# Optimization experiments

Measured on AMD Instinct MI355X. Metric: run time of the kernel, lower is better.

## Reference

```python
import jax, jax.numpy as jnp
import numpy as np

LN_EPS = 1e-5
BOUNDARY_ID = 0  # boundary_ids = {space_id} = {0}


def setup_inputs() -> dict:
    key = jax.random.key(0)
    k1, k2, k3 = jax.random.split(key, 3)
    B, T, D = 16, 8192, 256
    x = jax.random.normal(k1, (B, T, D), dtype=jnp.float32)
    input_ids = jax.random.randint(k2, (B, T), 0, 8, dtype=jnp.int64)
    W_proj = jax.random.normal(k3, (D, D), dtype=jnp.float32) / np.sqrt(D)
    b_proj = jnp.zeros((D,), dtype=jnp.float32)
    gamma = jnp.ones((D,), dtype=jnp.float32)
    beta = jnp.zeros((D,), dtype=jnp.float32)
    return {"x": x, "input_ids": input_ids, "W_proj": W_proj,
            "b_proj": b_proj, "gamma": gamma, "beta": beta}


def _pool(x, input_ids):
    # Boundary-defined segment mean pooling, vectorized via segment_sum.
    B, T, D = x.shape
    boundary = input_ids == BOUNDARY_ID                       # [B,T]
    nonb = ~boundary
    # A segment starts at a non-boundary token at t=0 or right after a boundary.
    prev_is_b = jnp.concatenate(
        [jnp.ones((B, 1), dtype=bool), boundary[:, :-1]], axis=1)
    start = nonb & prev_is_b
    seg = jnp.cumsum(start.astype(jnp.int32), axis=1) - 1     # seg idx per token
    MAXW = T  # static upper bound on number of segments (jit-safe padding)
    row_off = jnp.arange(B, dtype=jnp.int32)[:, None] * MAXW
    dump = B * MAXW  # boundary tokens go to a dummy segment, dropped below
    flat_ids = jnp.where(nonb, seg + row_off, dump).reshape(-1)
    sums = jax.ops.segment_sum(x.reshape(-1, D), flat_ids,
                               num_segments=B * MAXW + 1)[:-1]
    counts = jax.ops.segment_sum(jnp.ones((B * T,), x.dtype), flat_ids,
                                 num_segments=B * MAXW + 1)[:-1]
    sums = sums.reshape(B, MAXW, D)
    counts = counts.reshape(B, MAXW)
    mask = (counts > 0).astype(x.dtype)                       # [B,MAXW]
    padded = sums / jnp.maximum(counts, 1.0)[..., None]       # zeros where empty
    return padded, mask


def reference(x, input_ids, W_proj, b_proj, gamma, beta):
    padded, mask = _pool(x, input_ids)
    out = jnp.einsum('bwd,ed->bwe', padded, W_proj) + b_proj  # nn.Linear
    mu = jnp.mean(out, axis=-1, keepdims=True)
    var = jnp.mean(jnp.square(out - mu), axis=-1, keepdims=True)
    out = (out - mu) * jax.lax.rsqrt(var + LN_EPS) * gamma + beta
    return out, mask
```

## Files before the change

### kernel.cpp

```cpp
#include <hip/hip_runtime.h>
#include <hip/hip_bf16.h>
#include <math.h>

#define BB 16
#define TT 8192
#define DD 256
#define MAXSEG 4096
#define RPB 8
#define LN_EPS 1e-5f

typedef float vfloat4 __attribute__((ext_vector_type(4)));

__global__ __launch_bounds__(1024) void setup_kernel(
    const int* __restrict__ ids, const float* __restrict__ W,
    const float* __restrict__ bp, const float* __restrict__ gamma,
    const float* __restrict__ beta, int* __restrict__ counts,
    int* __restrict__ seg_start, int* __restrict__ nseg_g,
    float* __restrict__ mask_out, float* __restrict__ Wt,
    float* __restrict__ ln_empty) {
    __shared__ int wtot_s[16];
    __shared__ int wtot_n[16];
    __shared__ int segs[MAXSEG];
    __shared__ int pvals[MAXSEG];

    int tid = threadIdx.x;
    int lane = tid & 63;
    int wv = tid >> 6;

    if (blockIdx.x >= BB) {
        int bi = blockIdx.x - BB;
        if (bi < 64) {
            int d = bi * 4 + (tid >> 8);
            int e = tid & 255;
            Wt[d * DD + e] = W[e * DD + d];
        } else if (wv == 0) {
            int e0 = lane * 4;
            float4 v = *(const float4*)(bp + e0);
            float s = v.x + v.y + v.z + v.w;
            float sq = v.x * v.x + v.y * v.y + v.z * v.z + v.w * v.w;
#pragma unroll
            for (int o = 32; o > 0; o >>= 1) {
                s += __shfl_down(s, o);
                sq += __shfl_down(sq, o);
            }
            s = __shfl(s, 0);
            sq = __shfl(sq, 0);
            float mu = s * (1.f / (float)DD);
            float var = sq * (1.f / (float)DD) - mu * mu;
            float rs = rsqrtf(fmaxf(var, 0.f) + LN_EPS);
            float4 ge = *(const float4*)(gamma + e0);
            float4 be = *(const float4*)(beta + e0);
            float4 o4;
            o4.x = (v.x - mu) * rs * ge.x + be.x;
            o4.y = (v.y - mu) * rs * ge.y + be.y;
            o4.z = (v.z - mu) * rs * ge.z + be.z;
            o4.w = (v.w - mu) * rs * ge.w + be.w;
            *(float4*)(ln_empty + e0) = o4;
        }
        return;
    }

    const int TPT = 8;
    int b = blockIdx.x;
    const int* row = ids + b * TT;
    int t0 = tid * TPT;

    int4 q0 = ((const int4*)(row + t0))[0];
    int4 q1 = ((const int4*)(row + t0))[1];
    int v[TPT] = {q0.x, q0.y, q0.z, q0.w, q1.x, q1.y, q1.z, q1.w};
    int prev = (tid == 0) ? 0 : row[t0 - 1];

    bool nb[TPT], st[TPT];
    int cstart = 0, cnon = 0;
#pragma unroll
    for (int j = 0; j < TPT; ++j) {
        nb[j] = (v[j] != 0);
        int pv = (j == 0) ? prev : v[j - 1];
        st[j] = nb[j] && (pv == 0);
        cstart += st[j] ? 1 : 0;
        cnon += nb[j] ? 1 : 0;
    }

    int ss = cstart, sn = cnon;
#pragma unroll
    for (int o = 1; o < 64; o <<= 1) {
        int us = __shfl_up(ss, o);
        int un = __shfl_up(sn, o);
        if (lane >= o) { ss += us; sn += un; }
    }
    if (lane == 63) { wtot_s[wv] = ss; wtot_n[wv] = sn; }
    __syncthreads();

    int bs = 0, bn = 0, tot_s = 0, tot_n = 0;
#pragma unroll
    for (int j = 0; j < 16; ++j) {
        int a = wtot_s[j], c = wtot_n[j];
        if (j < wv) { bs += a; bn += c; }
        tot_s += a; tot_n += c;
    }
    bs += ss - cstart;
    bn += sn - cnon;

#pragma unroll
    for (int j = 0; j < TPT; ++j) {
        if (st[j]) { segs[bs] = t0 + j; pvals[bs] = bn; bs++; }
        bn += nb[j] ? 1 : 0;
    }
    __syncthreads();

    int ns = tot_s;
    for (int w = tid; w < TT; w += 1024) {
        int c = 0;
        if (w < ns) {
            int pe = (w + 1 < ns) ? pvals[w + 1] : tot_n;
            c = pe - pvals[w];
            seg_start[b * TT + w] = segs[w];
        }
        counts[b * TT + w] = c;
        mask_out[b * TT + w] = (w < ns) ? 1.0f : 0.0f;
    }
    if (tid == 0) nseg_g[b] = ns;
}

__global__ __launch_bounds__(256) void fused_kernel(
    const float* __restrict__ x, const float* __restrict__ Wt,
    const float* __restrict__ bp, const float* __restrict__ gamma,
    const float* __restrict__ beta, const int* __restrict__ counts,
    const int* __restrict__ seg_start, const int* __restrict__ nseg,
    const float* __restrict__ ln_e, float* __restrict__ out) {
    __shared__ float pooled[RPB][DD];
    __shared__ float red[4][RPB][2];

    int b = blockIdx.x;
    int wbase = blockIdx.y * RPB;
    int ns = nseg[b];
    int tid = threadIdx.x;
    int lane = tid & 63;
    int wv = tid >> 6;
    size_t rowbase = ((size_t)(b * TT + wbase)) * DD;

    if (wbase >= ns) {
        vfloat4 lv = *(const vfloat4*)(ln_e + 4 * lane);
        float* o = out + rowbase + 4 * lane;
#pragma unroll
        for (int rr = 0; rr < 2; ++rr) {
            int row = wv * 2 + rr;
            __builtin_nontemporal_store(lv, (vfloat4*)(o + (size_t)row * DD));
        }
        return;
    }
    int nr = min(RPB, ns - wbase);

#pragma unroll
    for (int rr = 0; rr < 2; ++rr) {
        int row = wv * 2 + rr;
        vfloat4 r = {0.f, 0.f, 0.f, 0.f};
        if (row < nr) {
            int w = wbase + row;
            int s = seg_start[b * TT + w];
            int len = counts[b * TT + w];
            const vfloat4* xp =
                (const vfloat4*)(x + ((size_t)(b * TT + s)) * DD) + lane;
            vfloat4 a[8];
#pragma unroll
            for (int j = 0; j < 8; ++j) a[j] = (vfloat4){0.f, 0.f, 0.f, 0.f};
            int t = 0;
            for (; t + 8 <= len; t += 8) {
#pragma unroll
                for (int j = 0; j < 8; ++j)
                    a[j] += __builtin_nontemporal_load(xp + (t + j) * 64);
            }
#pragma unroll
            for (int j = 0; j < 7; ++j)
                if (t + j < len)
                    a[j] += __builtin_nontemporal_load(xp + (t + j) * 64);
            r = ((a[0] + a[1]) + (a[2] + a[3])) + ((a[4] + a[5]) + (a[6] + a[7]));
            r *= (1.f / (float)len);
        }
        *(vfloat4*)&pooled[row][lane * 4] = r;
    }
    __syncthreads();

    int c = wv * 64 + lane;
    float acc[RPB];
    float bias = bp[c];
#pragma unroll
    for (int r = 0; r < RPB; ++r) acc[r] = bias;

    const float* Wc = Wt + c;
    float w0 = Wc[0 * DD];
    float w1 = Wc[1 * DD];
    float w2 = Wc[2 * DD];
    float w3 = Wc[3 * DD];
#pragma unroll 1
    for (int d0 = 0; d0 < DD; d0 += 4) {
        int dn = (d0 + 4) & 255;
        float n0 = Wc[(dn + 0) * DD];
        float n1 = Wc[(dn + 1) * DD];
        float n2 = Wc[(dn + 2) * DD];
        float n3 = Wc[(dn + 3) * DD];
#pragma unroll
        for (int r = 0; r < RPB; ++r) {
            const float4 p = *(const float4*)&pooled[r][d0];
            acc[r] = fmaf(p.x, w0, acc[r]);
            acc[r] = fmaf(p.y, w1, acc[r]);
            acc[r] = fmaf(p.z, w2, acc[r]);
            acc[r] = fmaf(p.w, w3, acc[r]);
        }
        w0 = n0; w1 = n1; w2 = n2; w3 = n3;
    }

#pragma unroll
    for (int r = 0; r < RPB; ++r) {
        float s = acc[r];
        float sq = acc[r] * acc[r];
#pragma unroll
        for (int o = 32; o > 0; o >>= 1) {
            s += __shfl_down(s, o);
            sq += __shfl_down(sq, o);
        }
        if (lane == 0) { red[wv][r][0] = s; red[wv][r][1] = sq; }
    }
    __syncthreads();

    float ga = gamma[c], be = beta[c];
#pragma unroll
    for (int r = 0; r < RPB; ++r) {
        float s = red[0][r][0] + red[1][r][0] + red[2][r][0] + red[3][r][0];
        float sq = red[0][r][1] + red[1][r][1] + red[2][r][1] + red[3][r][1];
        float mu = s * (1.f / (float)DD);
        float var = sq * (1.f / (float)DD) - mu * mu;
        float rs = rsqrtf(fmaxf(var, 0.f) + LN_EPS);
        float v = (acc[r] - mu) * rs * ga + be;
        __builtin_nontemporal_store(v, out + rowbase + (size_t)r * DD + c);
    }
}

extern "C" void kernel_launch(void* const* d_in, const int* in_sizes, int n_in,
                              void* d_out, int out_size, void* d_ws, size_t ws_size,
                              hipStream_t stream) {
    const float* x = (const float*)d_in[0];
    const int* ids = (const int*)d_in[1];
    const float* W = (const float*)d_in[2];
    const float* bp = (const float*)d_in[3];
    const float* gamma = (const float*)d_in[4];
    const float* beta = (const float*)d_in[5];

    float* out = (float*)d_out;
    float* mask = out + (size_t)BB * TT * DD;

    char* ws = (char*)d_ws;
    int* counts = (int*)ws;
    int* seg_start = (int*)(ws + (size_t)BB * TT * 4);
    int* nseg = (int*)(ws + (size_t)2 * BB * TT * 4);
    float* Wt = (float*)(ws + (size_t)2 * BB * TT * 4 + 256);
    float* ln_e = Wt + DD * DD;

    hipLaunchKernelGGL(setup_kernel, dim3(BB + 64 + 1), dim3(1024), 0, stream,
                       ids, W, bp, gamma, beta, counts, seg_start, nseg, mask,
                       Wt, ln_e);
    hipLaunchKernelGGL(fused_kernel, dim3(BB, TT / RPB), dim3(256), 0, stream,
                       x, Wt, bp, gamma, beta, counts, seg_start, nseg, ln_e, out);
}
```

Baseline: 269.6 us.

## Split fused pool+GEMM kernel into separate pooling and GEMM kernels

Breaks the single fused kernel into a pooling/fill kernel that writes pooled rows to a workspace buffer and a GEMM+LayerNorm kernel that reads them back. The GEMM loop now reads pooled values straight from global memory with 8-wide W register blocking. If the workspace is too small, it falls back to fusing the pooling into the GEMM kernel. The aim is to separate the memory-bound pooling from the compute phase so that neither stalls the other. The cost is an extra kernel launch plus a round trip of the pooled data through global memory.

```diff
diff --git a/kernel.cpp b/kernel.cpp
--- a/kernel.cpp
+++ b/kernel.cpp
@@ -122,24 +122,20 @@
     if (tid == 0) nseg_g[b] = ns;
 }
 
-__global__ __launch_bounds__(256) void fused_kernel(
-    const float* __restrict__ x, const float* __restrict__ Wt,
-    const float* __restrict__ bp, const float* __restrict__ gamma,
-    const float* __restrict__ beta, const int* __restrict__ counts,
+__global__ __launch_bounds__(256) void pool_fill_kernel(
+    const float* __restrict__ x, const int* __restrict__ counts,
     const int* __restrict__ seg_start, const int* __restrict__ nseg,
-    const float* __restrict__ ln_e, float* __restrict__ out) {
-    __shared__ float pooled[RPB][DD];
-    __shared__ float red[4][RPB][2];
-
+    const float* __restrict__ ln_e, float* __restrict__ pooled,
+    float* __restrict__ out, int capW) {
     int b = blockIdx.x;
     int wbase = blockIdx.y * RPB;
     int ns = nseg[b];
     int tid = threadIdx.x;
     int lane = tid & 63;
     int wv = tid >> 6;
-    size_t rowbase = ((size_t)(b * TT + wbase)) * DD;
 
     if (wbase >= ns) {
+        size_t rowbase = ((size_t)(b * TT + wbase)) * DD;
         vfloat4 lv = *(const vfloat4*)(ln_e + 4 * lane);
         float* o = out + rowbase + 4 * lane;
 #pragma unroll
@@ -149,6 +145,7 @@
         }
         return;
     }
+    if (wbase + RPB > capW) return;
     int nr = min(RPB, ns - wbase);
 
 #pragma unroll
@@ -177,37 +174,105 @@
             r = ((a[0] + a[1]) + (a[2] + a[3])) + ((a[4] + a[5]) + (a[6] + a[7]));
             r *= (1.f / (float)len);
         }
-        *(vfloat4*)&pooled[row][lane * 4] = r;
-    }
-    __syncthreads();
-
-    int c = wv * 64 + lane;
+        *(vfloat4*)(pooled + ((size_t)b * capW + wbase + wv * 2 + rr) * DD +
+                    4 * lane) = r;
+    }
+}
+
+__global__ __launch_bounds__(256) void gemm_kernel(
+    const float* __restrict__ x, const float* __restrict__ Wt,
+    const float* __restrict__ bp, const float* __restrict__ gamma,
+    const float* __restrict__ beta, const int* __restrict__ counts,
+    const int* __restrict__ seg_start, const int* __restrict__ nseg,
+    const float* __restrict__ pooled, float* __restrict__ out, int capW) {
+    __shared__ float pl[RPB][DD];
+    __shared__ float red[4][RPB][2];
+
+    int b = blockIdx.x;
+    int wbase = blockIdx.y * RPB;
+    int ns = nseg[b];
+    if (wbase >= ns) return;
+    int tid = threadIdx.x;
+    int lane = tid & 63;
+    int wv = tid >> 6;
+    int nr = min(RPB, ns - wbase);
+    size_t rowbase = ((size_t)(b * TT + wbase)) * DD;
+
+    int c = tid;
+    float bias = bp[c];
     float acc[RPB];
-    float bias = bp[c];
 #pragma unroll
     for (int r = 0; r < RPB; ++r) acc[r] = bias;
 
-    const float* Wc = Wt + c;
-    float w0 = Wc[0 * DD];
-    float w1 = Wc[1 * DD];
-    float w2 = Wc[2 * DD];
-    float w3 = Wc[3 * DD];
+    if (wbase + RPB <= capW) {
+        const float* __restrict__ pr = pooled + ((size_t)b * capW + wbase) * DD;
+        const float* __restrict__ Wc = Wt + c;
 #pragma unroll 1
-    for (int d0 = 0; d0 < DD; d0 += 4) {
-        int dn = (d0 + 4) & 255;
-        float n0 = Wc[(dn + 0) * DD];
-        float n1 = Wc[(dn + 1) * DD];
-        float n2 = Wc[(dn + 2) * DD];
-        float n3 = Wc[(dn + 3) * DD];
-#pragma unroll
-        for (int r = 0; r < RPB; ++r) {
-            const float4 p = *(const float4*)&pooled[r][d0];
-            acc[r] = fmaf(p.x, w0, acc[r]);
-            acc[r] = fmaf(p.y, w1, acc[r]);
-            acc[r] = fmaf(p.z, w2, acc[r]);
-            acc[r] = fmaf(p.w, w3, acc[r]);
-        }
-        w0 = n0; w1 = n1; w2 = n2; w3 = n3;
+        for (int d0 = 0; d0 < DD; d0 += 8) {
+            float w[8];
+#pragma unroll
+            for (int j = 0; j < 8; ++j) w[j] = Wc[(d0 + j) * DD];
+#pragma unroll
+            for (int r = 0; r < RPB; ++r) {
+#pragma unroll
+                for (int j = 0; j < 8; ++j)
+                    acc[r] = fmaf(pr[r * DD + d0 + j], w[j], acc[r]);
+            }
+        }
+    } else {
+#pragma unroll
+        for (int rr = 0; rr < 2; ++rr) {
+            int row = wv * 2 + rr;
+            vfloat4 r = {0.f, 0.f, 0.f, 0.f};
+            if (row < nr) {
+                int w = wbase + row;
+                int s = seg_start[b * TT + w];
+                int len = counts[b * TT + w];
+                const vfloat4* xp =
+                    (const vfloat4*)(x + ((size_t)(b * TT + s)) * DD) + lane;
+                vfloat4 a[8];
+#pragma unroll
+                for (int j = 0; j < 8; ++j) a[j] = (vfloat4){0.f, 0.f, 0.f, 0.f};
+                int t = 0;
+                for (; t + 8 <= len; t += 8) {
+#pragma unroll
+                    for (int j = 0; j < 8; ++j)
+                        a[j] += __builtin_nontemporal_load(xp + (t + j) * 64);
+                }
+#pragma unroll
+                for (int j = 0; j < 7; ++j)
+                    if (t + j < len)
+                        a[j] += __builtin_nontemporal_load(xp + (t + j) * 64);
+                r = ((a[0] + a[1]) + (a[2] + a[3])) +
+                    ((a[4] + a[5]) + (a[6] + a[7]));
+                r *= (1.f / (float)len);
+            }
+            *(vfloat4*)&pl[row][lane * 4] = r;
+        }
+        __syncthreads();
+
+        const float* Wc = Wt + c;
+        float w0 = Wc[0 * DD];
+        float w1 = Wc[1 * DD];
+        float w2 = Wc[2 * DD];
+        float w3 = Wc[3 * DD];
+#pragma unroll 1
+        for (int d0 = 0; d0 < DD; d0 += 4) {
+            int dn = (d0 + 4) & 255;
+            float n0 = Wc[(dn + 0) * DD];
+            float n1 = Wc[(dn + 1) * DD];
+            float n2 = Wc[(dn + 2) * DD];
+            float n3 = Wc[(dn + 3) * DD];
+#pragma unroll
+            for (int r = 0; r < RPB; ++r) {
+                const float4 p = *(const float4*)&pl[r][d0];
+                acc[r] = fmaf(p.x, w0, acc[r]);
+                acc[r] = fmaf(p.y, w1, acc[r]);
+                acc[r] = fmaf(p.z, w2, acc[r]);
+                acc[r] = fmaf(p.w, w3, acc[r]);
+            }
+            w0 = n0; w1 = n1; w2 = n2; w3 = n3;
+        }
     }
 
 #pragma unroll
@@ -255,10 +320,20 @@
     int* nseg = (int*)(ws + (size_t)2 * BB * TT * 4);
     float* Wt = (float*)(ws + (size_t)2 * BB * TT * 4 + 256);
     float* ln_e = Wt + DD * DD;
+    float* pooled = ln_e + 256;
+    size_t base = (size_t)2 * BB * TT * 4 + 256 + (size_t)DD * DD * 4 + 1024;
+    size_t avail = (ws_size > base) ? (ws_size - base) : 0;
+    long capW = (long)(avail / ((size_t)BB * DD * 4));
+    if (capW > MAXSEG) capW = MAXSEG;
+    capW &= ~(long)(RPB - 1);
 
     hipLaunchKernelGGL(setup_kernel, dim3(BB + 64 + 1), dim3(1024), 0, stream,
                        ids, W, bp, gamma, beta, counts, seg_start, nseg, mask,
                        Wt, ln_e);
-    hipLaunchKernelGGL(fused_kernel, dim3(BB, TT / RPB), dim3(256), 0, stream,
-                       x, Wt, bp, gamma, beta, counts, seg_start, nseg, ln_e, out);
+    hipLaunchKernelGGL(pool_fill_kernel, dim3(BB, TT / RPB), dim3(256), 0,
+                       stream, x, counts, seg_start, nseg, ln_e, pooled, out,
+                       (int)capW);
+    hipLaunchKernelGGL(gemm_kernel, dim3(BB, MAXSEG / RPB), dim3(256), 0,
+                       stream, x, Wt, bp, gamma, beta, counts, seg_start, nseg,
+                       pooled, out, (int)capW);
 }
```

Result: slower. 307.6 us (+14.1%).

## Process 32 pooled rows per block to amortize projection weight reads

Applied to the files above, without the earlier changes.

The fused kernel now has one block in every group of four pool 32 segment rows and run the projection and LayerNorm on all of them. The other three blocks, whose rows are already covered, exit early. Each weight column loaded from L2 is reused across 32 rows instead of 8, which cuts the repeated full-matrix weight traffic. In exchange each thread holds 32 accumulators, which raises register pressure. Pooling parallelism also drops, since fewer active blocks serialize four pooling passes, and the launched grid still includes the idle blocks.

```diff
diff --git a/kernel.cpp b/kernel.cpp
--- a/kernel.cpp
+++ b/kernel.cpp
@@ -7,6 +7,7 @@
 #define DD 256
 #define MAXSEG 4096
 #define RPB 8
+#define LROWS 32
 #define LN_EPS 1e-5f
 
 typedef float vfloat4 __attribute__((ext_vector_type(4)));
@@ -128,8 +129,8 @@
     const float* __restrict__ beta, const int* __restrict__ counts,
     const int* __restrict__ seg_start, const int* __restrict__ nseg,
     const float* __restrict__ ln_e, float* __restrict__ out) {
-    __shared__ float pooled[RPB][DD];
-    __shared__ float red[4][RPB][2];
+    __shared__ float pooled[LROWS][DD];
+    __shared__ float red[LROWS][4][2];
 
     int b = blockIdx.x;
     int wbase = blockIdx.y * RPB;
@@ -137,9 +138,9 @@
     int tid = threadIdx.x;
     int lane = tid & 63;
     int wv = tid >> 6;
-    size_t rowbase = ((size_t)(b * TT + wbase)) * DD;
 
     if (wbase >= ns) {
+        size_t rowbase = ((size_t)(b * TT + wbase)) * DD;
         vfloat4 lv = *(const vfloat4*)(ln_e + 4 * lane);
         float* o = out + rowbase + 4 * lane;
 #pragma unroll
@@ -149,49 +150,56 @@
         }
         return;
     }
-    int nr = min(RPB, ns - wbase);
-
-#pragma unroll
-    for (int rr = 0; rr < 2; ++rr) {
-        int row = wv * 2 + rr;
-        vfloat4 r = {0.f, 0.f, 0.f, 0.f};
-        if (row < nr) {
-            int w = wbase + row;
-            int s = seg_start[b * TT + w];
-            int len = counts[b * TT + w];
-            const vfloat4* xp =
-                (const vfloat4*)(x + ((size_t)(b * TT + s)) * DD) + lane;
-            vfloat4 a[8];
-#pragma unroll
-            for (int j = 0; j < 8; ++j) a[j] = (vfloat4){0.f, 0.f, 0.f, 0.f};
-            int t = 0;
-            for (; t + 8 <= len; t += 8) {
-#pragma unroll
-                for (int j = 0; j < 8; ++j)
-                    a[j] += __builtin_nontemporal_load(xp + (t + j) * 64);
+    if (wbase & (LROWS - 1)) return;
+    int nr = min(LROWS, ns - wbase);
+
+#pragma unroll 1
+    for (int pr = 0; pr < 4; ++pr) {
+#pragma unroll
+        for (int rr = 0; rr < 2; ++rr) {
+            int row = wv * 8 + pr * 2 + rr;
+            vfloat4 r = {0.f, 0.f, 0.f, 0.f};
+            if (row < nr) {
+                int w = wbase + row;
+                int s = seg_start[b * TT + w];
+                int len = counts[b * TT + w];
+                const vfloat4* xp =
+                    (const vfloat4*)(x + ((size_t)(b * TT + s)) * DD) + lane;
+                vfloat4 a[8];
+#pragma unroll
+                for (int j = 0; j < 8; ++j) a[j] = (vfloat4){0.f, 0.f, 0.f, 0.f};
+                int t = 0;
+                for (; t + 8 <= len; t += 8) {
+#pragma unroll
+                    for (int j = 0; j < 8; ++j)
+                        a[j] += __builtin_nontemporal_load(xp + (t + j) * 64);
+                }
+#pragma unroll
+                for (int j = 0; j < 7; ++j)
+                    if (t + j < len)
+                        a[j] += __builtin_nontemporal_load(xp + (t + j) * 64);
+                r = ((a[0] + a[1]) + (a[2] + a[3])) +
+                    ((a[4] + a[5]) + (a[6] + a[7]));
+                r *= (1.f / (float)len);
             }
-#pragma unroll
-            for (int j = 0; j < 7; ++j)
-                if (t + j < len)
-                    a[j] += __builtin_nontemporal_load(xp + (t + j) * 64);
-            r = ((a[0] + a[1]) + (a[2] + a[3])) + ((a[4] + a[5]) + (a[6] + a[7]));
-            r *= (1.f / (float)len);
-        }
-        *(vfloat4*)&pooled[row][lane * 4] = r;
-    }
-    __syncthreads();
-
-    int c = wv * 64 + lane;
-    float acc[RPB];
-    float bias = bp[c];
-#pragma unroll
-    for (int r = 0; r < RPB; ++r) acc[r] = bias;
-
+            *(vfloat4*)&pooled[row][lane * 4] = r;
+        }
+    }
+
+    int c = tid;
     const float* Wc = Wt + c;
     float w0 = Wc[0 * DD];
     float w1 = Wc[1 * DD];
     float w2 = Wc[2 * DD];
     float w3 = Wc[3 * DD];
+    float bias = bp[c];
+
+    __syncthreads();
+
+    float acc[LROWS];
+#pragma unroll
+    for (int r = 0; r < LROWS; ++r) acc[r] = bias;
+
 #pragma unroll 1
     for (int d0 = 0; d0 < DD; d0 += 4) {
         int dn = (d0 + 4) & 255;
@@ -200,7 +208,7 @@
         float n2 = Wc[(dn + 2) * DD];
         float n3 = Wc[(dn + 3) * DD];
 #pragma unroll
-        for (int r = 0; r < RPB; ++r) {
+        for (int r = 0; r < LROWS; ++r) {
             const float4 p = *(const float4*)&pooled[r][d0];
             acc[r] = fmaf(p.x, w0, acc[r]);
             acc[r] = fmaf(p.y, w1, acc[r]);
@@ -211,7 +219,7 @@
     }
 
 #pragma unroll
-    for (int r = 0; r < RPB; ++r) {
+    for (int r = 0; r < LROWS; ++r) {
         float s = acc[r];
         float sq = acc[r] * acc[r];
 #pragma unroll
@@ -219,15 +227,18 @@
             s += __shfl_down(s, o);
             sq += __shfl_down(sq, o);
         }
-        if (lane == 0) { red[wv][r][0] = s; red[wv][r][1] = sq; }
+        if (lane == 0) { red[r][wv][0] = s; red[r][wv][1] = sq; }
     }
     __syncthreads();
 
     float ga = gamma[c], be = beta[c];
-#pragma unroll
-    for (int r = 0; r < RPB; ++r) {
-        float s = red[0][r][0] + red[1][r][0] + red[2][r][0] + red[3][r][0];
-        float sq = red[0][r][1] + red[1][r][1] + red[2][r][1] + red[3][r][1];
+    size_t rowbase = ((size_t)(b * TT + wbase)) * DD;
+#pragma unroll
+    for (int r = 0; r < LROWS; ++r) {
+        float4 q0 = *(const float4*)&red[r][0][0];
+        float4 q1 = *(const float4*)&red[r][2][0];
+        float s = (q0.x + q0.z) + (q1.x + q1.z);
+        float sq = (q0.y + q0.w) + (q1.y + q1.w);
         float mu = s * (1.f / (float)DD);
         float var = sq * (1.f / (float)DD) - mu * mu;
         float rs = rsqrtf(fmaxf(var, 0.f) + LN_EPS);
```

Measured after the change: 333.4 us. 1.24x slower.
